# Kernel optimization log

Hardware: AMD Instinct MI355X
Metric: run time of the kernel (lower is better)

The kernel has to match this reference:

```python
import jax, jax.numpy as jnp
import numpy as np

PAD = 4          # pad_size == max_displacement
K = 1            # avgpool kernel_size
S1, S2 = 1, 1    # avgpool strides


def _avg_pool(x, k, s1, s2):
    # x: [B, C, H, W]; AvgPool2d(k, stride=(s1, s2)) with VALID padding
    if k == 1 and s1 == 1 and s2 == 1:
        return x
    summed = jax.lax.reduce_window(
        x, 0.0, jax.lax.add,
        window_dimensions=(1, 1, k, k),
        window_strides=(1, 1, s1, s2),
        padding='VALID')
    return summed / float(k * k)


def setup_inputs() -> dict:
    key = jax.random.key(0)
    k1, k2 = jax.random.split(key)
    shape = (8, 196, 128, 224)
    input1 = jax.random.normal(k1, shape, dtype=jnp.float32)
    input2 = jax.random.normal(k2, shape, dtype=jnp.float32)
    return {"input1": input1, "input2": input2}


def reference(input1, input2):
    B, C, H, W = input1.shape
    # reflect-pad input2 spatially by PAD on each side
    x2 = jnp.pad(input2, ((0, 0), (0, 0), (PAD, PAD), (PAD, PAD)), mode='reflect')
    corrs = []
    for hi in range(2 * PAD + 1):        # fixed small displacement set (9x9)
        for wi in range(2 * PAD + 1):
            shifted = jax.lax.dynamic_slice(x2, (0, 0, hi, wi), (B, C, H, W))
            prod = input1 * shifted                      # [B,C,H,W]
            pooled = _avg_pool(prod, K, S1, S2)          # [B,C,H',W']
            corrs.append(jnp.sum(pooled, axis=1) / C)    # [B,H',W']
    return jnp.stack(corrs, axis=1)                      # [B,81,H',W']
```

## Files before the change

kernel.cpp:

```cpp
#include <hip/hip_runtime.h>


constexpr int NB = 8, NC = 196, NH = 128, NW = 224;
constexpr int ND = 9;
constexpr int PADV = 4;
constexpr int WS = 232;
constexpr int KC = 2;
constexpr int NSLOT = 56;
constexpr int ACTIVE = ND * NSLOT;
constexpr int TPB = 512;
constexpr int HWSZ = NH * NW;

__device__ __forceinline__ int refl(int v, int n) {
    v = v < 0 ? -v : v;
    return v >= n ? 2 * n - 2 - v : v;
}

__global__ __launch_bounds__(TPB)
void corr_kernel(const float* __restrict__ in1,
                 const float* __restrict__ in2,
                 float* __restrict__ out)
{
    __shared__ float s_win[KC][ND][WS];

    const int tid = threadIdx.x;
    const int bh  = blockIdx.x;
    const int b   = bh / NH;
    const int h   = bh - b * NH;

    const float* gA[2];
    int  lA[2];
    bool vA[2];
#pragma unroll
    for (int k = 0; k < 2; ++k) {
        int v  = tid + k * TPB;
        vA[k]  = v < KC * ND * NSLOT;
        int vv = vA[k] ? v : 0;
        int cc = vv / (ND * NSLOT);
        int r  = vv - cc * (ND * NSLOT);
        int dh = r / NSLOT;
        int g  = r - dh * NSLOT;
        int y  = refl(h + dh - PADV, NH);
        gA[k]  = in2 + ((b * NC + cc) * NH + y) * NW + 4 * g;
        lA[k]  = (cc * ND + dh) * WS + 4 + 4 * g;
    }
    const float* gB = in2;
    int  lB = 0;
    const bool vB = tid < KC * ND * 8;
    {
        int v  = vB ? tid : 0;
        int cc = v / (ND * 8);
        int r  = v - cc * (ND * 8);
        int dh = r / 8;
        int e  = r - dh * 8;
        int s  = e < 4 ? e : 224 + e;
        int x  = e < 4 ? 4 - e : 226 - e;
        int y  = refl(h + dh - PADV, NH);
        gB = in2 + ((b * NC + cc) * NH + y) * NW + x;
        lB = (cc * ND + dh) * WS + s;
    }

    const int  cdh  = tid / NSLOT;
    const int  slot = tid - cdh * NSLOT;
    const int  w0   = slot * 4;
    const bool compute = tid < ACTIVE;
    const float* a1p = in1 + ((b * NC) * NH + h) * NW + w0;

    float acc[ND][4];
#pragma unroll
    for (int d = 0; d < ND; ++d)
#pragma unroll
        for (int p = 0; p < 4; ++p) acc[d][p] = 0.f;

    float4 bufA[2];
    float  bufB = 0.f;
#pragma unroll
    for (int k = 0; k < 2; ++k)
        if (vA[k]) bufA[k] = *(const float4*)(gA[k]);
    if (vB) bufB = gB[0];

    for (int c0 = 0; c0 < NC; c0 += KC) {
        __syncthreads();
#pragma unroll
        for (int k = 0; k < 2; ++k)
            if (vA[k]) *(float4*)&((float*)s_win)[lA[k]] = bufA[k];
        if (vB) ((float*)s_win)[lB] = bufB;
        __syncthreads();

        const int c1 = c0 + KC;
        if (c1 < NC) {
            const int off = c1 * HWSZ;
#pragma unroll
            for (int k = 0; k < 2; ++k)
                if (vA[k]) bufA[k] = *(const float4*)(gA[k] + off);
            if (vB) bufB = gB[off];
        }

        if (compute) {
#pragma unroll
            for (int cc = 0; cc < KC; ++cc) {
                const float* wrow = &s_win[cc][cdh][w0];
                float4 wv0 = *(const float4*)(wrow);
                float4 wv1 = *(const float4*)(wrow + 4);
                float4 wv2 = *(const float4*)(wrow + 8);
                const float wn[12] = {wv0.x, wv0.y, wv0.z, wv0.w,
                                      wv1.x, wv1.y, wv1.z, wv1.w,
                                      wv2.x, wv2.y, wv2.z, wv2.w};
                float4 a = *(const float4*)(a1p + (c0 + cc) * HWSZ);
#pragma unroll
                for (int d = 0; d < ND; ++d) {
                    acc[d][0] += a.x * wn[d + 0];
                    acc[d][1] += a.y * wn[d + 1];
                    acc[d][2] += a.z * wn[d + 2];
                    acc[d][3] += a.w * wn[d + 3];
                }
            }
        }
    }

    if (compute) {
        const float scale = 1.0f / 196.0f;
#pragma unroll
        for (int d = 0; d < ND; ++d) {
            float4 o;
            o.x = acc[d][0] * scale;
            o.y = acc[d][1] * scale;
            o.z = acc[d][2] * scale;
            o.w = acc[d][3] * scale;
            float* op = out + (((b * (ND * ND)) + cdh * ND + d) * NH + h) * NW + w0;
            *(float4*)op = o;
        }
    }
}

extern "C" void kernel_launch(void* const* d_in, const int* in_sizes, int n_in,
                              void* d_out, int out_size, void* d_ws, size_t ws_size,
                              hipStream_t stream)
{
    const float* in1 = (const float*)d_in[0];
    const float* in2 = (const float*)d_in[1];
    float* outp = (float*)d_out;
    dim3 grid(NB * NH);
    dim3 block(TPB);
    hipLaunchKernelGGL(corr_kernel, grid, block, 0, stream, in1, in2, outp);
}
```

Baseline: 659.5 us.

## Double-buffer shared window, single barrier per step, XCD-aware block remap

Makes the shared-memory window double-buffered so each channel step needs one barrier instead of two, and the next tile is stored while the current one is consumed. Blocks are also remapped so that consecutive rows of the same batch land on the same XCD, for better L2 reuse of the overlapping reflected rows. The row stride is padded from 232 to 236 floats to change the LDS bank mapping. Shared memory use doubles, which may reduce occupancy.

```diff
diff --git a/kernel.cpp b/kernel.cpp
--- a/kernel.cpp
+++ b/kernel.cpp
@@ -4,12 +4,15 @@
 constexpr int NB = 8, NC = 196, NH = 128, NW = 224;
 constexpr int ND = 9;
 constexpr int PADV = 4;
-constexpr int WS = 232;
+constexpr int WS = 236;
 constexpr int KC = 2;
 constexpr int NSLOT = 56;
 constexpr int ACTIVE = ND * NSLOT;
 constexpr int TPB = 512;
 constexpr int HWSZ = NH * NW;
+constexpr int NR = NC / KC;
+constexpr int NXCD = 8;
+constexpr int NBLK = NB * NH;
 
 __device__ __forceinline__ int refl(int v, int n) {
     v = v < 0 ? -v : v;
@@ -21,10 +24,10 @@
                  const float* __restrict__ in2,
                  float* __restrict__ out)
 {
-    __shared__ float s_win[KC][ND][WS];
+    __shared__ __align__(16) float s_win[2][KC][ND][WS];
 
     const int tid = threadIdx.x;
-    const int bh  = blockIdx.x;
+    const int bh = (blockIdx.x & (NXCD - 1)) * (NBLK / NXCD) + (blockIdx.x >> 3);
     const int b   = bh / NH;
     const int h   = bh - b * NH;
 
@@ -78,35 +81,33 @@
     for (int k = 0; k < 2; ++k)
         if (vA[k]) bufA[k] = *(const float4*)(gA[k]);
     if (vB) bufB = gB[0];
-
-    for (int c0 = 0; c0 < NC; c0 += KC) {
-        __syncthreads();
+    {
+        float* dst = &s_win[0][0][0][0];
 #pragma unroll
         for (int k = 0; k < 2; ++k)
-            if (vA[k]) *(float4*)&((float*)s_win)[lA[k]] = bufA[k];
-        if (vB) ((float*)s_win)[lB] = bufB;
-        __syncthreads();
+            if (vA[k]) *(float4*)(dst + lA[k]) = bufA[k];
+        if (vB) dst[lB] = bufB;
+    }
+#pragma unroll
+    for (int k = 0; k < 2; ++k)
+        if (vA[k]) bufA[k] = *(const float4*)(gA[k] + KC * HWSZ);
+    if (vB) bufB = gB[KC * HWSZ];
+    __syncthreads();
 
-        const int c1 = c0 + KC;
-        if (c1 < NC) {
-            const int off = c1 * HWSZ;
-#pragma unroll
-            for (int k = 0; k < 2; ++k)
-                if (vA[k]) bufA[k] = *(const float4*)(gA[k] + off);
-            if (vB) bufB = gB[off];
-        }
+    for (int r = 0; r < NR; ++r) {
+        const int cur = r & 1;
 
         if (compute) {
 #pragma unroll
             for (int cc = 0; cc < KC; ++cc) {
-                const float* wrow = &s_win[cc][cdh][w0];
+                const float* wrow = &s_win[cur][cc][cdh][w0];
                 float4 wv0 = *(const float4*)(wrow);
                 float4 wv1 = *(const float4*)(wrow + 4);
                 float4 wv2 = *(const float4*)(wrow + 8);
                 const float wn[12] = {wv0.x, wv0.y, wv0.z, wv0.w,
                                       wv1.x, wv1.y, wv1.z, wv1.w,
                                       wv2.x, wv2.y, wv2.z, wv2.w};
-                float4 a = *(const float4*)(a1p + (c0 + cc) * HWSZ);
+                float4 a = *(const float4*)(a1p + (r * KC + cc) * HWSZ);
 #pragma unroll
                 for (int d = 0; d < ND; ++d) {
                     acc[d][0] += a.x * wn[d + 0];
@@ -116,6 +117,22 @@
                 }
             }
         }
+
+        if (r + 1 < NR) {
+            float* dst = &s_win[cur ^ 1][0][0][0];
+#pragma unroll
+            for (int k = 0; k < 2; ++k)
+                if (vA[k]) *(float4*)(dst + lA[k]) = bufA[k];
+            if (vB) dst[lB] = bufB;
+            if (r + 2 < NR) {
+                const int off = (r + 2) * KC * HWSZ;
+#pragma unroll
+                for (int k = 0; k < 2; ++k)
+                    if (vA[k]) bufA[k] = *(const float4*)(gA[k] + off);
+                if (vB) bufB = gB[off];
+            }
+        }
+        __syncthreads();
     }
 
     if (compute) {
@@ -140,7 +157,7 @@
     const float* in1 = (const float*)d_in[0];
     const float* in2 = (const float*)d_in[1];
     float* outp = (float*)d_out;
-    dim3 grid(NB * NH);
+    dim3 grid(NBLK);
     dim3 block(TPB);
     hipLaunchKernelGGL(corr_kernel, grid, block, 0, stream, in1, in2, outp);
 }
```

Measured after the change: 830.9 us. +26.0%, slower.
